# Optimization experiments

Measured on AMD Instinct MI355X. Metric: run time of the kernel, lower is better.

## Reference

```python
import jax, jax.numpy as jnp
import numpy as np
from jax import lax

S, B, D = 512, 64, 120          # seq_len, batch, input_dim
OC, K = 16, 6                   # conv out_channels, kernel_size
H, O = 1024, 48                 # lstm hidden, output_dim
AFTER_CONV = (D - K) + 1        # 115 (stride=1, pad=0, dil=1)
AFTER_POOL = AFTER_CONV - 1     # 114 (maxpool k=2, stride=1)
LSTM_IN = AFTER_POOL * OC       # 1824


def setup_inputs() -> dict:
    key = jax.random.key(0)
    ks = jax.random.split(key, 12)
    inp = {
        "input_": jax.random.normal(ks[0], (S, B, D), dtype=jnp.float32),
        "hidden": jnp.zeros((1, B, H), dtype=jnp.float32),
        "cell": jnp.zeros((1, B, H), dtype=jnp.float32),
        "conv_w": jax.random.normal(ks[1], (OC, 1, K), dtype=jnp.float32) * 0.1,
        "conv_b": jax.random.normal(ks[2], (OC,), dtype=jnp.float32) * 0.1,
        "w_ih": jax.random.normal(ks[3], (4 * H, LSTM_IN), dtype=jnp.float32) * 0.02,
        "w_hh": jax.random.normal(ks[4], (4 * H, H), dtype=jnp.float32) * 0.02,
        "b_ih": jax.random.normal(ks[5], (4 * H,), dtype=jnp.float32) * 0.02,
        "b_hh": jax.random.normal(ks[6], (4 * H,), dtype=jnp.float32) * 0.02,
        "h2h_w": jax.random.normal(ks[7], (H, H), dtype=jnp.float32) * 0.02,
        "h2h_b": jax.random.normal(ks[8], (H,), dtype=jnp.float32) * 0.02,
        "out_w": jax.random.normal(ks[9], (O, H), dtype=jnp.float32) * 0.02,
        "out_b": jax.random.normal(ks[10], (O,), dtype=jnp.float32) * 0.02,
    }
    return inp


def _forward(input_, hidden, cell, conv_w, conv_b, w_ih, w_hh, b_ih, b_hh,
             h2h_w, h2h_b, out_w, out_b):
    s, b, d = input_.shape
    # in_channels=1 -> context_len=0: per-step conv == batched conv over [S*B, 1, D]
    x = input_.reshape(s * b, 1, d)
    c = lax.conv_general_dilated(x, conv_w, window_strides=(1,), padding="VALID",
                                 dimension_numbers=("NCH", "OIH", "NCH"))
    c = jax.nn.relu(c + conv_b[None, :, None])            # [S*B, OC, AFTER_CONV]
    p = jnp.maximum(c[:, :, :-1], c[:, :, 1:])            # maxpool k=2 stride=1
    feat = p.reshape(s, b, -1)                            # [S, B, OC*AFTER_POOL]

    def step(carry, x_t):
        h, cst = carry
        gates = x_t @ w_ih.T + b_ih + h @ w_hh.T + b_hh   # [B, 4H]
        i, f, g, o = jnp.split(gates, 4, axis=-1)          # torch gate order i,f,g,o
        i = jax.nn.sigmoid(i); f = jax.nn.sigmoid(f)
        g = jnp.tanh(g); o = jax.nn.sigmoid(o)
        cst = f * cst + i * g
        h = o * jnp.tanh(cst)
        return (h, cst), h

    (_, _), hs = lax.scan(step, (hidden[0], cell[0]), feat)  # hs: [S, B, H]
    hs = jax.nn.relu(hs)
    h2 = jax.nn.relu(hs @ h2h_w.T + h2h_b)                # [S, B, H]
    logits = h2 @ out_w.T + out_b                         # [S, B, O]
    return jax.nn.log_softmax(logits, axis=-1)


def reference(input_, hidden, cell, conv_w, conv_b, w_ih, w_hh, b_ih, b_hh,
              h2h_w, h2h_b, out_w, out_b):
    return _forward(input_, hidden, cell, conv_w, conv_b, w_ih, w_hh, b_ih, b_hh,
                    h2h_w, h2h_b, out_w, out_b)
```

## Files before the change

kernel.cpp:

```cpp
#include <hip/hip_runtime.h>
#include <stdint.h>
#include <stddef.h>

#define kS 512
#define kB 64
#define kD 120
#define kOC 16
#define kKSZ 6
#define kPOOL 114
#define kLIN 1824
#define kH 1024
#define kG 4096
#define kO 48
#define kROWS (kS * kB)
#define RNB 256
#define SLOT 16384

typedef __attribute__((ext_vector_type(8))) short bf16x8;
typedef __attribute__((ext_vector_type(4))) float f32x4;

__device__ __forceinline__ unsigned short f32_to_bf16(float f) {
  unsigned u = __float_as_uint(f);
  u += 0x7FFFu + ((u >> 16) & 1u);
  return (unsigned short)(u >> 16);
}
__device__ __forceinline__ float bf16_to_f32(unsigned short h) {
  return __uint_as_float(((unsigned)h) << 16);
}
__device__ __forceinline__ float sigmoid_(float x) { return 1.f / (1.f + __expf(-x)); }
__device__ __forceinline__ float tanh_(float x) { return 1.f - 2.f / (__expf(2.f * x) + 1.f); }

__device__ __forceinline__ void load_lds_16(const void* g, void* l) {
  __builtin_amdgcn_global_load_lds((__attribute__((address_space(1))) void*)g,
                                   (__attribute__((address_space(3))) void*)l, 16, 0, 0);
}

__device__ __forceinline__ void bar_lgkm() {
  __builtin_amdgcn_sched_barrier(0);
  asm volatile("s_waitcnt lgkmcnt(0)" ::: "memory");
  __builtin_amdgcn_s_barrier();
  __builtin_amdgcn_sched_barrier(0);
}

__device__ __forceinline__ unsigned long long coh_load(const unsigned long long* p) {
  return __hip_atomic_load(p, __ATOMIC_RELAXED, __HIP_MEMORY_SCOPE_AGENT);
}
__device__ __forceinline__ void coh_store(unsigned long long* p, unsigned long long v) {
  __hip_atomic_store(p, v, __ATOMIC_RELAXED, __HIP_MEMORY_SCOPE_AGENT);
}
__device__ __forceinline__ int inval(unsigned long long q) {
  return ((q >> 7) & 0xFFull) == 0xFEull;
}

__global__ void convert_weights(const float* __restrict__ wih, const float* __restrict__ whh,
                                const float* __restrict__ h2hw, const float* __restrict__ outw,
                                const float* __restrict__ bih, const float* __restrict__ bhh,
                                unsigned short* __restrict__ wihb, unsigned short* __restrict__ whhb,
                                unsigned short* __restrict__ h2hwb, unsigned short* __restrict__ outwb,
                                float* __restrict__ bsum) {
  const size_t N0 = (size_t)kG * kLIN;
  const size_t N1 = (size_t)kG * kH;
  const size_t N2 = (size_t)kH * kH;
  const size_t N3 = (size_t)kO * kH;
  const size_t N4 = kG;
  const size_t TOT = N0 + N1 + N2 + N3 + N4;
  for (size_t i = (size_t)blockIdx.x * blockDim.x + threadIdx.x; i < TOT;
       i += (size_t)gridDim.x * blockDim.x) {
    if (i < N0) wihb[i] = f32_to_bf16(wih[i]);
    else if (i < N0 + N1) whhb[i - N0] = f32_to_bf16(whh[i - N0]);
    else if (i < N0 + N1 + N2) h2hwb[i - N0 - N1] = f32_to_bf16(h2hw[i - N0 - N1]);
    else if (i < N0 + N1 + N2 + N3) outwb[i - N0 - N1 - N2] = f32_to_bf16(outw[i - N0 - N1 - N2]);
    else { size_t j = i - N0 - N1 - N2 - N3; bsum[j] = bih[j] + bhh[j]; }
  }
}

__global__ __launch_bounds__(256) void conv_pool(const float* __restrict__ x,
                                                 const float* __restrict__ cw,
                                                 const float* __restrict__ cb,
                                                 unsigned short* __restrict__ feat,
                                                 long row_base) {
  __shared__ float xs[8][kD];
  __shared__ float ws[kOC][kKSZ];
  __shared__ float bs[kOC];
  const int tid = threadIdx.x;
  const long grow0 = row_base + (long)blockIdx.x * 8;
  const long lrow0 = (long)blockIdx.x * 8;
  if (tid < kOC * kKSZ) ws[tid / kKSZ][tid % kKSZ] = cw[tid];
  if (tid < kOC) bs[tid] = cb[tid];
  for (int i = tid; i < 8 * kD; i += 256) xs[i / kD][i % kD] = x[grow0 * kD + i];
  __syncthreads();
  for (int r = 0; r < 8; ++r) {
    for (int idx = tid; idx < kLIN; idx += 256) {
      const int oc = idx / kPOOL, p = idx % kPOOL;
      float c0 = bs[oc], c1 = bs[oc];
#pragma unroll
      for (int k = 0; k < kKSZ; ++k) {
        c0 += xs[r][p + k] * ws[oc][k];
        c1 += xs[r][p + 1 + k] * ws[oc][k];
      }
      float v = fmaxf(fmaxf(c0, c1), 0.f);
      feat[(lrow0 + r) * kLIN + idx] = f32_to_bf16(v);
    }
  }
}

template <int MODE>
__global__ __launch_bounds__(256) void gemm_bt_bf16(const unsigned short* __restrict__ A,
                                                    const unsigned short* __restrict__ B,
                                                    const float* __restrict__ bias,
                                                    unsigned short* __restrict__ C,
                                                    int N, int K) {
  __shared__ unsigned short Al[2][128 * 32];
  __shared__ unsigned short Bl[2][128 * 32];
  const int tid = threadIdx.x;
  const int lane = tid & 63;
  const int wid = tid >> 6;
  const int wm = wid >> 1, wn = wid & 1;
  const long bm = (long)blockIdx.x * 128;
  const long bn = (long)blockIdx.y * 128;
  const int NT = K / 32;

  f32x4 acc[4][4] = {};

  auto stage = [&](int buf, int kt) {
    const long k0 = (long)kt * 32;
#pragma unroll
    for (int rnd = 0; rnd < 2; ++rnd) {
      const int chunk = rnd * 256 + tid;
      const int r = chunk >> 2, c = chunk & 3;
      load_lds_16(A + (bm + r) * K + k0 + c * 8, &Al[buf][chunk * 8]);
      load_lds_16(B + (bn + r) * K + k0 + c * 8, &Bl[buf][chunk * 8]);
    }
  };

  stage(0, 0);
  __syncthreads();
  int buf = 0;
  for (int kt = 0; kt < NT; ++kt) {
    if (kt + 1 < NT) stage(buf ^ 1, kt + 1);
    bf16x8 af[4], bfr[4];
#pragma unroll
    for (int i = 0; i < 4; ++i) {
      const int ar = wm * 64 + i * 16 + (lane & 15);
      af[i] = *(const bf16x8*)&Al[buf][ar * 32 + (lane >> 4) * 8];
      const int bc = wn * 64 + i * 16 + (lane & 15);
      bfr[i] = *(const bf16x8*)&Bl[buf][bc * 32 + (lane >> 4) * 8];
    }
#pragma unroll
    for (int i = 0; i < 4; ++i)
#pragma unroll
      for (int j = 0; j < 4; ++j)
        acc[i][j] = __builtin_amdgcn_mfma_f32_16x16x32_bf16(af[i], bfr[j], acc[i][j], 0, 0, 0);
    __syncthreads();
    buf ^= 1;
  }

#pragma unroll
  for (int i = 0; i < 4; ++i) {
#pragma unroll
    for (int j = 0; j < 4; ++j) {
      const long col = bn + wn * 64 + j * 16 + (lane & 15);
      const float bv = bias[col];
#pragma unroll
      for (int e = 0; e < 4; ++e) {
        const long row = bm + wm * 64 + i * 16 + (lane >> 4) * 4 + e;
        float v = acc[i][j][e] + bv;
        if (MODE == 1) v = fmaxf(v, 0.f);
        if (MODE == 2) {
          const int g = (int)(col >> 10), ub = (int)((col >> 4) & 63), ur = (int)(col & 15);
          C[(row * 64 + ub) * 64 + g * 16 + ur] = f32_to_bf16(v);
        } else {
          C[row * N + col] = f32_to_bf16(v);
        }
      }
    }
  }
}

__global__ __launch_bounds__(512) void lstm_rec(const unsigned short* __restrict__ xw,
                                                const unsigned short* __restrict__ whh,
                                                const float* __restrict__ h0,
                                                const float* __restrict__ c0,
                                                float* __restrict__ cst,
                                                unsigned long long* __restrict__ hbuf,
                                                unsigned short* __restrict__ hs,
                                                int nsteps, int first, int t0step) {
  __shared__ unsigned short Bl[64 * 1024];
  __shared__ unsigned short hstage[256];
  __shared__ unsigned pacc_h[8][2][4][64];
  const int tid = threadIdx.x;
  const int lane = tid & 63;
  const int kq = tid >> 6;
  const int urow = lane & 15;
  const int bq = lane >> 4;
  const int bid = blockIdx.x;
  const int ublk = bid & 63;
  const int bqtr = bid >> 6;
  const int u0 = ublk * 16;
  const bool gatewave = (kq < 4);
  const int gbL = bq * 4 + kq;
  const int gbW = bqtr * 16 + gbL;

  for (int idx = tid; idx < 64 * 128; idx += 512) {
    const int col = idx & 63;
    const int kc = idx >> 6;
    const int gcol = (col >> 4) * kH + u0 + (col & 15);
    *(bf16x8*)&Bl[kc * 512 + col * 8] = *(const bf16x8*)&whh[(long)gcol * kH + kc * 8];
  }
  float creg = 0.f;
  if (first) {
    if (tid < 64) {
      const int lb = tid >> 2, un4 = (tid & 3) * 4, gb = bqtr * 16 + lb;
      unsigned long long v = 0;
#pragma unroll
      for (int e = 0; e < 4; ++e) {
        const unsigned long long b16 = f32_to_bf16(h0[gb * kH + u0 + un4 + e]);
        v |= b16 << (16 * e);
      }
      coh_store(&hbuf[(size_t)ublk * 256 + gb * 4 + (tid & 3)], v);
    }
    if (gatewave) creg = c0[gbW * kH + u0 + urow];
  } else {
    if (gatewave) creg = cst[gbW * kH + u0 + urow];
  }
  bar_lgkm();

  float xv[4];
  auto load_xv = [&](int t) {
    const unsigned short* xp = xw + ((long)(t * kB + gbW) * 64 + ublk) * 64 + urow;
#pragma unroll
    for (int g = 0; g < 4; ++g) xv[g] = bf16_to_f32(xp[g * 16]);
  };
  if (gatewave) load_xv(0);

  const int ach = (bqtr * 16 + urow) * 4 + (bq & 1) * 2;

  for (int t = 0; t < nsteps; ++t) {
    const unsigned long long* curs = hbuf + (size_t)(t0step + t) * SLOT;
    unsigned long long* nxts = hbuf + (size_t)(t0step + t + 1) * SLOT;

    unsigned long long q[8];
#pragma unroll
    for (int i = 0; i < 8; ++i)
      q[i] = coh_load(curs + (size_t)((kq * 4 + (i >> 1)) * 2 + (bq >> 1)) * 256 + ach + (i & 1));
    for (;;) {
      int bad = 0;
#pragma unroll
      for (int i = 0; i < 8; ++i) bad |= inval(q[i]);
      if (!bad) break;
      unsigned long long t2[8];
#pragma unroll
      for (int i = 0; i < 8; ++i)
        t2[i] =
            coh_load(curs + (size_t)((kq * 4 + (i >> 1)) * 2 + (bq >> 1)) * 256 + ach + (i & 1));
#pragma unroll
      for (int i = 0; i < 8; ++i) q[i] = t2[i];
    }

    f32x4 acc[4] = {};
#pragma unroll
    for (int ktl = 0; ktl < 4; ++ktl) {
      union { unsigned long long qq[2]; bf16x8 v; } a;
      a.qq[0] = q[2 * ktl];
      a.qq[1] = q[2 * ktl + 1];
      const int kc = (kq * 4 + ktl) * 4 + bq;
#pragma unroll
      for (int g = 0; g < 4; ++g) {
        const bf16x8 bb = *(const bf16x8*)&Bl[kc * 512 + (g * 16 + urow) * 8];
        acc[g] = __builtin_amdgcn_mfma_f32_16x16x32_bf16(a.v, bb, acc[g], 0, 0, 0);
      }
    }

#pragma unroll
    for (int j = 0; j < 4; ++j)
#pragma unroll
      for (int gp = 0; gp < 2; ++gp) {
        const unsigned lo = f32_to_bf16(acc[2 * gp][j]);
        const unsigned hi = f32_to_bf16(acc[2 * gp + 1][j]);
        pacc_h[kq][gp][j][lane] = lo | (hi << 16);
      }
    bar_lgkm();

    if (gatewave) {
      float s[4] = {xv[0], xv[1], xv[2], xv[3]};
#pragma unroll
      for (int p = 0; p < 8; ++p) {
        const unsigned v0 = pacc_h[p][0][kq][lane];
        const unsigned v1 = pacc_h[p][1][kq][lane];
        s[0] += bf16_to_f32((unsigned short)v0);
        s[1] += bf16_to_f32((unsigned short)(v0 >> 16));
        s[2] += bf16_to_f32((unsigned short)v1);
        s[3] += bf16_to_f32((unsigned short)(v1 >> 16));
      }
      const float gi = sigmoid_(s[0]);
      const float gf = sigmoid_(s[1]);
      const float gg = tanh_(s[2]);
      const float go = sigmoid_(s[3]);
      creg = gf * creg + gi * gg;
      hstage[gbL * 16 + urow] = f32_to_bf16(go * tanh_(creg));
      asm volatile("" ::: "memory");
      if (lane < 16) {
        const int lb = (lane >> 2) * 4 + kq;
        const int e = lane & 3;
        unsigned long long qp = 0;
#pragma unroll
        for (int x = 0; x < 4; ++x)
          qp |= ((unsigned long long)hstage[lb * 16 + e * 4 + x]) << (16 * x);
        coh_store(&nxts[(size_t)ublk * 256 + (bqtr * 16 + lb) * 4 + e], qp);
        unsigned long long r = 0;
#pragma unroll
        for (int x = 0; x < 4; ++x) {
          unsigned long long sv = (qp >> (16 * x)) & 0xFFFFull;
          if (sv & 0x8000ull) sv = 0;
          r |= sv << (16 * x);
        }
        *(unsigned long long*)&hs[(long)(t * kB + bqtr * 16 + lb) * kH + u0 + e * 4] = r;
      }
      if (t + 1 < nsteps) load_xv(t + 1);
    }
    bar_lgkm();
  }

  if (gatewave) cst[gbW * kH + u0 + urow] = creg;
}

__global__ __launch_bounds__(256) void out_head(const unsigned short* __restrict__ h2,
                                                const unsigned short* __restrict__ ow,
                                                const float* __restrict__ ob,
                                                float* __restrict__ out) {
  __shared__ unsigned short Wl[48 * 1024];
  const int tid = threadIdx.x;
  const int lane = tid & 63;
  const int w = tid >> 6;
  for (int idx = tid; idx < 48 * 128; idx += 256) {
    const int col = idx % 48;
    const int kc = idx / 48;
    *(bf16x8*)&Wl[kc * 384 + col * 8] = *(const bf16x8*)&ow[(long)col * kH + kc * 8];
  }
  __syncthreads();
  const long row0 = (long)blockIdx.x * 64 + w * 16;
  f32x4 acc[3] = {};
  const unsigned short* arow = h2 + (row0 + (lane & 15)) * kH + (lane >> 4) * 8;
#pragma unroll 8
  for (int kt = 0; kt < 32; ++kt) {
    const bf16x8 a = *(const bf16x8*)(arow + kt * 32);
    const int kc = kt * 4 + (lane >> 4);
#pragma unroll
    for (int n = 0; n < 3; ++n) {
      const bf16x8 bb = *(const bf16x8*)&Wl[kc * 384 + (n * 16 + (lane & 15)) * 8];
      acc[n] = __builtin_amdgcn_mfma_f32_16x16x32_bf16(a, bb, acc[n], 0, 0, 0);
    }
  }
  const int colb = lane & 15;
#pragma unroll
  for (int j = 0; j < 4; ++j) {
    float v[3];
#pragma unroll
    for (int n = 0; n < 3; ++n) v[n] = acc[n][j] + ob[n * 16 + colb];
    float m = fmaxf(fmaxf(v[0], v[1]), v[2]);
#pragma unroll
    for (int s = 1; s < 16; s <<= 1) m = fmaxf(m, __shfl_xor(m, s, 64));
    float se = __expf(v[0] - m) + __expf(v[1] - m) + __expf(v[2] - m);
#pragma unroll
    for (int s = 1; s < 16; s <<= 1) se += __shfl_xor(se, s, 64);
    const float lse = m + __logf(se);
    const long row = row0 + (lane >> 4) * 4 + j;
#pragma unroll
    for (int n = 0; n < 3; ++n) out[row * 48 + n * 16 + colb] = v[n] - lse;
  }
}

extern "C" void kernel_launch(void* const* d_in, const int* in_sizes, int n_in,
                              void* d_out, int out_size, void* d_ws, size_t ws_size,
                              hipStream_t stream) {
  const float* input_ = (const float*)d_in[0];
  const float* hidden = (const float*)d_in[1];
  const float* cell = (const float*)d_in[2];
  const float* conv_w = (const float*)d_in[3];
  const float* conv_b = (const float*)d_in[4];
  const float* w_ih = (const float*)d_in[5];
  const float* w_hh = (const float*)d_in[6];
  const float* b_ih = (const float*)d_in[7];
  const float* b_hh = (const float*)d_in[8];
  const float* h2h_w = (const float*)d_in[9];
  const float* h2h_b = (const float*)d_in[10];
  const float* out_w = (const float*)d_in[11];
  const float* out_b = (const float*)d_in[12];
  float* out = (float*)d_out;

  const size_t HBUF_BYTES = (size_t)(kS + 1) * SLOT * 8;

  const size_t FIXED = ((size_t)kG * kLIN + (size_t)kG * kH + (size_t)kH * kH +
                        (size_t)kO * kH) * 2 +
                       (size_t)kG * 4 +
                       HBUF_BYTES +
                       (size_t)kB * kH * 4 +
                       16 * 256;

  int CHUNK = 2;
  const int cand[] = {512, 256, 128, 64, 32, 16, 8, 4, 2};
  for (int i = 0; i < 9; ++i) {
    const size_t rowsC = (size_t)cand[i] * kB;
    const size_t need = FIXED + rowsC * (kLIN + kG) * 2;
    if (need <= ws_size) { CHUNK = cand[i]; break; }
  }
  const size_t rowsC = (size_t)CHUNK * kB;

  char* ws = (char*)d_ws;
  size_t off = 0;
  auto alloc = [&](size_t bytes) {
    char* p = ws + off;
    off += (bytes + 255) & ~(size_t)255;
    return p;
  };
  unsigned short* regionA = (unsigned short*)alloc(rowsC * kLIN * 2);
  unsigned short* regionB = (unsigned short*)alloc(rowsC * kG * 2);
  unsigned short* wih_b = (unsigned short*)alloc((size_t)kG * kLIN * 2);
  unsigned short* whh_b = (unsigned short*)alloc((size_t)kG * kH * 2);
  unsigned short* h2hw_b = (unsigned short*)alloc((size_t)kH * kH * 2);
  unsigned short* outw_b = (unsigned short*)alloc((size_t)kO * kH * 2);
  float* bias_sum = (float*)alloc((size_t)kG * 4);
  unsigned long long* hbuf = (unsigned long long*)alloc(HBUF_BYTES);
  float* cstate = (float*)alloc((size_t)kB * kH * 4);

  unsigned short* feat_c = regionA;
  unsigned short* hs_c = regionA;
  unsigned short* xw_c = regionB;
  unsigned short* h2_c = regionB;

  hipMemsetAsync(hbuf, 0x7F, HBUF_BYTES, stream);
  convert_weights<<<2048, 256, 0, stream>>>(w_ih, w_hh, h2h_w, out_w, b_ih, b_hh, wih_b, whh_b,
                                            h2hw_b, outw_b, bias_sum);

  const int nch = kS / CHUNK;
  for (int ci = 0; ci < nch; ++ci) {
    const long t0 = (long)ci * CHUNK;
    conv_pool<<<(int)(rowsC / 8), 256, 0, stream>>>(input_, conv_w, conv_b, feat_c, t0 * kB);
    gemm_bt_bf16<2><<<dim3((int)(rowsC / 128), kG / 128), 256, 0, stream>>>(
        feat_c, wih_b, bias_sum, xw_c, kG, kLIN);
    lstm_rec<<<RNB, 512, 0, stream>>>(xw_c, whh_b, hidden, cell, cstate, hbuf, hs_c, CHUNK,
                                      ci == 0 ? 1 : 0, (int)t0);
    gemm_bt_bf16<1><<<dim3((int)(rowsC / 128), kH / 128), 256, 0, stream>>>(
        hs_c, h2hw_b, h2h_b, h2_c, kH, kH);
    out_head<<<(int)(rowsC / 64), 256, 0, stream>>>(h2_c, outw_b, out_b, out + t0 * kB * kO);
  }
}
```

Before: 2.181 ms.

## Add 256x256 pipelined input-projection GEMM with K padded to 1920

Replaces the 128x128 tile GEMM for the LSTM input projection with a 256x256, 512-thread kernel. It stages 64-wide K slices in a double-buffered LDS pipeline with fine-grained waitcnt and barriers, and raises priority around the MFMA blocks. The input-feature dimension is zero-padded from 1824 to 1920 in both the weights and the conv output so K divides into 128-wide iterations. The padding adds some extra FLOPs and memory, and the minimum chunk size rises to 4 timesteps.

After: 2.017 ms. 7.5% less time.

```diff
diff --git a/kernel.cpp b/kernel.cpp
--- a/kernel.cpp
+++ b/kernel.cpp
@@ -9,6 +9,7 @@
 #define kKSZ 6
 #define kPOOL 114
 #define kLIN 1824
+#define kLINP 1920
 #define kH 1024
 #define kG 4096
 #define kO 48
@@ -58,7 +59,7 @@
                                 unsigned short* __restrict__ wihb, unsigned short* __restrict__ whhb,
                                 unsigned short* __restrict__ h2hwb, unsigned short* __restrict__ outwb,
                                 float* __restrict__ bsum) {
-  const size_t N0 = (size_t)kG * kLIN;
+  const size_t N0 = (size_t)kG * kLINP;
   const size_t N1 = (size_t)kG * kH;
   const size_t N2 = (size_t)kH * kH;
   const size_t N3 = (size_t)kO * kH;
@@ -66,8 +67,11 @@
   const size_t TOT = N0 + N1 + N2 + N3 + N4;
   for (size_t i = (size_t)blockIdx.x * blockDim.x + threadIdx.x; i < TOT;
        i += (size_t)gridDim.x * blockDim.x) {
-    if (i < N0) wihb[i] = f32_to_bf16(wih[i]);
-    else if (i < N0 + N1) whhb[i - N0] = f32_to_bf16(whh[i - N0]);
+    if (i < N0) {
+      const size_t row = i / kLINP;
+      const int col = (int)(i % kLINP);
+      wihb[i] = (col < kLIN) ? f32_to_bf16(wih[row * kLIN + col]) : 0;
+    } else if (i < N0 + N1) whhb[i - N0] = f32_to_bf16(whh[i - N0]);
     else if (i < N0 + N1 + N2) h2hwb[i - N0 - N1] = f32_to_bf16(h2hw[i - N0 - N1]);
     else if (i < N0 + N1 + N2 + N3) outwb[i - N0 - N1 - N2] = f32_to_bf16(outw[i - N0 - N1 - N2]);
     else { size_t j = i - N0 - N1 - N2 - N3; bsum[j] = bih[j] + bhh[j]; }
@@ -99,12 +103,13 @@
         c1 += xs[r][p + 1 + k] * ws[oc][k];
       }
       float v = fmaxf(fmaxf(c0, c1), 0.f);
-      feat[(lrow0 + r) * kLIN + idx] = f32_to_bf16(v);
-    }
-  }
-}
-
-template <int MODE>
+      feat[(lrow0 + r) * kLINP + idx] = f32_to_bf16(v);
+    }
+    for (int idx = kLIN + tid; idx < kLINP; idx += 256)
+      feat[(lrow0 + r) * kLINP + idx] = 0;
+  }
+}
+
 __global__ __launch_bounds__(256) void gemm_bt_bf16(const unsigned short* __restrict__ A,
                                                     const unsigned short* __restrict__ B,
                                                     const float* __restrict__ bias,
@@ -164,14 +169,109 @@
 #pragma unroll
       for (int e = 0; e < 4; ++e) {
         const long row = bm + wm * 64 + i * 16 + (lane >> 4) * 4 + e;
-        float v = acc[i][j][e] + bv;
-        if (MODE == 1) v = fmaxf(v, 0.f);
-        if (MODE == 2) {
-          const int g = (int)(col >> 10), ub = (int)((col >> 4) & 63), ur = (int)(col & 15);
-          C[(row * 64 + ub) * 64 + g * 16 + ur] = f32_to_bf16(v);
-        } else {
-          C[row * N + col] = f32_to_bf16(v);
-        }
+        C[row * N + col] = f32_to_bf16(fmaxf(acc[i][j][e] + bv, 0.f));
+      }
+    }
+  }
+}
+
+__global__ __launch_bounds__(512, 2) void gemm256_m2(const unsigned short* __restrict__ A,
+                                                     const unsigned short* __restrict__ B,
+                                                     const float* __restrict__ bias,
+                                                     unsigned short* __restrict__ C,
+                                                     int Kp) {
+  __shared__ unsigned short AL[2][2][128 * 64];
+  __shared__ unsigned short BL[2][2][128 * 64];
+  const int tid = threadIdx.x;
+  const int lane = tid & 63;
+  const int wid = tid >> 6;
+  const int wm = wid >> 2;
+  const int wn = wid & 3;
+  const long bm = (long)blockIdx.x * 256;
+  const long bn = (long)blockIdx.y * 256;
+  const int iters = Kp / 128;
+  const int nkt = iters * 2;
+
+  f32x4 acc[8][4] = {};
+
+  auto stageu = [&](int db, int op, int hf, int kt) {
+    const unsigned short* S = op ? B : A;
+    const long base = op ? bn : bm;
+    unsigned short* L = op ? &BL[db][hf][0] : &AL[db][hf][0];
+#pragma unroll
+    for (int c = 0; c < 2; ++c) {
+      const int ch = c * 512 + tid;
+      const int r = ch >> 3;
+      const int cb = (ch & 7) * 8;
+      load_lds_16(S + (base + hf * 128 + r) * Kp + (long)kt * 64 + cb, L + r * 64 + cb);
+    }
+  };
+
+#pragma unroll
+  for (int kt = 0; kt < 2; ++kt)
+#pragma unroll
+    for (int u = 0; u < 4; ++u) stageu(0, u >> 1, u & 1, kt);
+  __builtin_amdgcn_sched_barrier(0);
+  asm volatile("s_waitcnt vmcnt(0)" ::: "memory");
+  __builtin_amdgcn_s_barrier();
+  __builtin_amdgcn_sched_barrier(0);
+
+  int d = 0;
+  for (int it = 0; it < iters; ++it, d ^= 1) {
+    bf16x8 bfr[8];
+#pragma unroll
+    for (int p = 0; p < 8; ++p) {
+      const int q = p & 3;
+      const int kbase = (p >> 2) ? 1 : 0;
+      if (q == 0) {
+#pragma unroll
+        for (int nf = 0; nf < 4; ++nf)
+#pragma unroll
+          for (int ks = 0; ks < 2; ++ks)
+            bfr[nf * 2 + ks] = *(const bf16x8*)&BL[d][wn >> 1]
+                [((wn & 1) * 64 + nf * 16 + (lane & 15)) * 64 + ks * 32 + (lane >> 4) * 8];
+      }
+      bf16x8 afr[2][2];
+#pragma unroll
+      for (int m2 = 0; m2 < 2; ++m2)
+#pragma unroll
+        for (int ks = 0; ks < 2; ++ks)
+          afr[m2][ks] = *(const bf16x8*)&AL[d][wm]
+              [((q * 2 + m2) * 16 + (lane & 15)) * 64 + ks * 32 + (lane >> 4) * 8];
+      (void)kbase;
+      const int ktN = it * 2 + 2 + (p >> 2);
+      if (ktN < nkt) stageu(d ^ 1, q >> 1, q & 1, ktN);
+      if (p == 3 || p == 7) {
+        __builtin_amdgcn_sched_barrier(0);
+        asm volatile("s_waitcnt vmcnt(8)" ::: "memory");
+      }
+      __builtin_amdgcn_s_barrier();
+      __builtin_amdgcn_s_setprio(1);
+#pragma unroll
+      for (int m2 = 0; m2 < 2; ++m2)
+#pragma unroll
+        for (int nf = 0; nf < 4; ++nf)
+#pragma unroll
+          for (int ks = 0; ks < 2; ++ks)
+            acc[q * 2 + m2][nf] = __builtin_amdgcn_mfma_f32_16x16x32_bf16(
+                afr[m2][ks], bfr[nf * 2 + ks], acc[q * 2 + m2][nf], 0, 0, 0);
+      __builtin_amdgcn_s_setprio(0);
+      __builtin_amdgcn_s_barrier();
+    }
+  }
+
+
+#pragma unroll
+  for (int mf = 0; mf < 8; ++mf) {
+#pragma unroll
+    for (int nf = 0; nf < 4; ++nf) {
+      const long col = bn + wn * 64 + nf * 16 + (lane & 15);
+      const float bv = bias[col];
+      const int g = (int)(col >> 10), ub = (int)((col >> 4) & 63), ur = (int)(col & 15);
+#pragma unroll
+      for (int e = 0; e < 4; ++e) {
+        const long row = bm + wm * 128 + mf * 16 + (lane >> 4) * 4 + e;
+        C[(row * 64 + ub) * 64 + g * 16 + ur] = f32_to_bf16(acc[mf][nf][e] + bv);
       }
     }
   }
@@ -390,18 +490,18 @@
 
   const size_t HBUF_BYTES = (size_t)(kS + 1) * SLOT * 8;
 
-  const size_t FIXED = ((size_t)kG * kLIN + (size_t)kG * kH + (size_t)kH * kH +
+  const size_t FIXED = ((size_t)kG * kLINP + (size_t)kG * kH + (size_t)kH * kH +
                         (size_t)kO * kH) * 2 +
                        (size_t)kG * 4 +
                        HBUF_BYTES +
                        (size_t)kB * kH * 4 +
                        16 * 256;
 
-  int CHUNK = 2;
-  const int cand[] = {512, 256, 128, 64, 32, 16, 8, 4, 2};
-  for (int i = 0; i < 9; ++i) {
+  int CHUNK = 4;
+  const int cand[] = {512, 256, 128, 64, 32, 16, 8, 4};
+  for (int i = 0; i < 8; ++i) {
     const size_t rowsC = (size_t)cand[i] * kB;
-    const size_t need = FIXED + rowsC * (kLIN + kG) * 2;
+    const size_t need = FIXED + rowsC * (kLINP + kG) * 2;
     if (need <= ws_size) { CHUNK = cand[i]; break; }
   }
   const size_t rowsC = (size_t)CHUNK * kB;
@@ -413,9 +513,9 @@
     off += (bytes + 255) & ~(size_t)255;
     return p;
   };
-  unsigned short* regionA = (unsigned short*)alloc(rowsC * kLIN * 2);
+  unsigned short* regionA = (unsigned short*)alloc(rowsC * kLINP * 2);
   unsigned short* regionB = (unsigned short*)alloc(rowsC * kG * 2);
-  unsigned short* wih_b = (unsigned short*)alloc((size_t)kG * kLIN * 2);
+  unsigned short* wih_b = (unsigned short*)alloc((size_t)kG * kLINP * 2);
   unsigned short* whh_b = (unsigned short*)alloc((size_t)kG * kH * 2);
   unsigned short* h2hw_b = (unsigned short*)alloc((size_t)kH * kH * 2);
   unsigned short* outw_b = (unsigned short*)alloc((size_t)kO * kH * 2);
@@ -436,12 +536,12 @@
   for (int ci = 0; ci < nch; ++ci) {
     const long t0 = (long)ci * CHUNK;
     conv_pool<<<(int)(rowsC / 8), 256, 0, stream>>>(input_, conv_w, conv_b, feat_c, t0 * kB);
-    gemm_bt_bf16<2><<<dim3((int)(rowsC / 128), kG / 128), 256, 0, stream>>>(
-        feat_c, wih_b, bias_sum, xw_c, kG, kLIN);
+    gemm256_m2<<<dim3((int)(rowsC / 256), kG / 256), 512, 0, stream>>>(feat_c, wih_b, bias_sum,
+                                                                       xw_c, kLINP);
     lstm_rec<<<RNB, 512, 0, stream>>>(xw_c, whh_b, hidden, cell, cstate, hbuf, hs_c, CHUNK,
                                       ci == 0 ? 1 : 0, (int)t0);
-    gemm_bt_bf16<1><<<dim3((int)(rowsC / 128), kH / 128), 256, 0, stream>>>(
-        hs_c, h2hw_b, h2h_b, h2_c, kH, kH);
+    gemm_bt_bf16<<<dim3((int)(rowsC / 128), kH / 128), 256, 0, stream>>>(hs_c, h2hw_b, h2h_b,
+                                                                         h2_c, kH, kH);
     out_head<<<(int)(rowsC / 64), 256, 0, stream>>>(h2_c, outw_b, out_b, out + t0 * kB * kO);
   }
 }
```
